# Performance work log

Hardware: AMD Instinct MI355X
Metric: run time of the kernel (lower is better)

## Reference

```python
import jax, jax.numpy as jnp
import numpy as np

IMAGE_SIZE = 224  # self.image_size; dims are all equal to this so postprocess is one bilinear resize
EPS = 1e-12      # F.normalize default eps


def setup_inputs() -> dict:
    key = jax.random.key(0)
    k1, k2 = jax.random.split(key)
    embeddings = jax.random.normal(k1, (2, 9, 256, 48, 48), dtype=jnp.float32)
    # binary class masks in {0,1}; channel 0 (background) is recomputed inside forward
    prompt_masks = jax.random.randint(k2, (2, 8, 4, 48, 48), 0, 2).astype(jnp.float32)
    dims = jnp.full((2, 1, 2), IMAGE_SIZE, dtype=jnp.int32)  # all original sizes == image_size
    return {"embeddings": embeddings, "prompt_masks": prompt_masks, "dims": dims}


def reference(embeddings, prompt_masks, dims):
    B, M, D, H, W = embeddings.shape
    HW = H * W
    q = embeddings[:, 0]            # (B, D, H, W)  query
    s = embeddings[:, 1:]           # (B, M-1, D, H, W)  supports
    # F.normalize: x / max(||x||, eps) along the feature dim
    qn = q / jnp.maximum(jnp.sqrt(jnp.sum(q * q, axis=1, keepdims=True)), EPS)
    sn = s / jnp.maximum(jnp.sqrt(jnp.sum(s * s, axis=2, keepdims=True)), EPS)

    q2 = qn.reshape(B, D, HW).transpose(0, 2, 1)              # (B, Q, D)
    s2 = sn.reshape(B, M - 1, D, HW).transpose(0, 1, 3, 2)    # (B, M1, K, D)
    sim = jnp.einsum('bqd,bmkd->bqmk', q2, s2)                # (B, Q, M1, K) cosine sims

    # nearest-resize of prompt masks to compare_size==(H,W) is identity here (same size)
    N = prompt_masks.shape[2]
    pm = prompt_masks.reshape(B, M - 1, N, HW)
    background = (pm[:, :, 1:, :].sum(axis=2) == 0).astype(sim.dtype)  # (B, M1, HW)
    pm = pm.at[:, :, 0, :].set(background)

    neg_inf = jnp.array(-jnp.inf, sim.dtype)
    logits = []
    for n in range(N):  # small fixed class count
        cm = pm[:, :, n, :][:, None]                 # (B, 1, M1, K) broadcast over Q
        masked = jnp.where(cm == 0, neg_inf, sim)    # (B, Q, M1, K)
        logits.append(masked.reshape(B, HW, -1).max(axis=-1))  # (B, Q)
    logits = jnp.stack(logits, axis=1).reshape(B, N, H, W)

    # postprocess_masks: bilinear to image_size; all original sizes == image_size so the
    # per-image second interpolate is identity and padding amounts are zero.
    out = jax.image.resize(logits, (B, N, IMAGE_SIZE, IMAGE_SIZE), method='bilinear')
    # masks[:,0][masks[:,0]==-inf] = 0  (no-op here, kept for faithfulness)
    out = out.at[:, 0].set(jnp.where(jnp.isneginf(out[:, 0]), 0.0, out[:, 0]))
    return out
```

## Files before the change

### kernel.cpp

```cpp
#include <hip/hip_runtime.h>
#include <hip/hip_bf16.h>
#include <math.h>

#define BB 2
#define MM 9
#define MS 8
#define DD 256
#define HW 2304
#define NCLS 4
#define OUTR 224

typedef float floatx4 __attribute__((ext_vector_type(4)));
typedef __bf16 bf16x8 __attribute__((ext_vector_type(8)));
typedef unsigned short ushortx8 __attribute__((ext_vector_type(8)));

__device__ __forceinline__ unsigned enc_f(float f) {
    unsigned u = __float_as_uint(f);
    return (u & 0x80000000u) ? ~u : (u | 0x80000000u);
}
__device__ __forceinline__ float dec_f(unsigned k) {
    unsigned u = (k & 0x80000000u) ? (k & 0x7FFFFFFFu) : ~k;
    return __uint_as_float(u);
}

__global__ __launch_bounds__(256) void knorm(const float* __restrict__ emb,
                                             __hip_bfloat16* __restrict__ outp,
                                             unsigned* __restrict__ enc_logits) {
    __shared__ float tile[256][33];
    __shared__ float psum[8][32];
    __shared__ float sscale[32];
    const int bm   = blockIdx.y;
    const int pix0 = blockIdx.x * 32;
    const int tid  = threadIdx.x;

    int flat = (blockIdx.y * gridDim.x + blockIdx.x) * 256 + tid;
    if (flat < BB * NCLS * HW) enc_logits[flat] = 0u;

    const float* src = emb + (size_t)bm * DD * HW + pix0;
    {
        const int dr = tid >> 3;
        const int p4 = (tid & 7) * 4;
#pragma unroll
        for (int r = 0; r < 8; ++r) {
            int d = r * 32 + dr;
            floatx4 v = *(const floatx4*)(src + (size_t)d * HW + p4);
            float* t = &tile[d][p4];
            t[0] = v[0]; t[1] = v[1]; t[2] = v[2]; t[3] = v[3];
        }
    }
    __syncthreads();
    {
        const int pc = tid & 31;
        const int dr = tid >> 5;
        float ss = 0.f;
#pragma unroll
        for (int s = 0; s < 32; ++s) {
            float v = tile[dr * 32 + s][pc];
            ss += v * v;
        }
        psum[dr][pc] = ss;
    }
    __syncthreads();
    if (tid < 32) {
        float t = 0.f;
#pragma unroll
        for (int c = 0; c < 8; ++c) t += psum[c][tid];
        sscale[tid] = 1.0f / fmaxf(sqrtf(t), 1e-12f);
    }
    __syncthreads();
    __hip_bfloat16* dst = outp + (size_t)bm * HW * DD + (size_t)pix0 * DD;
#pragma unroll
    for (int r = 0; r < 32; ++r) {
        float v = tile[tid][r] * sscale[r];
        dst[(size_t)r * DD + tid] = __float2bfloat16(v);
    }
}

__device__ __forceinline__ void gld16(const unsigned short* g, unsigned short* l) {
    __builtin_amdgcn_global_load_lds((__attribute__((address_space(1))) void*)g,
                                     (__attribute__((address_space(3))) void*)l, 16, 0, 0);
}

#define BK 64
#define REDSTRIDE 132
#define SMEM_BYTES 33792

__global__ __launch_bounds__(256, 4) void kgemm(const unsigned short* __restrict__ normed,
                                                const float* __restrict__ pm,
                                                unsigned* __restrict__ enc_logits) {
    __shared__ __attribute__((aligned(16))) unsigned char smem[SMEM_BYTES];
    unsigned short* As = (unsigned short*)smem;
    unsigned short* Bs = As + 128 * 64;
    float* red = (float*)smem;

    const int ct = blockIdx.x;
    const int rt = blockIdx.y;
    const int b  = blockIdx.z;
    const int m  = ct / 18;
    const int kt = ct % 18;

    const int tid  = threadIdx.x;
    const int lane = tid & 63;
    const int wave = tid >> 6;
    const int wr = wave >> 1, wc = wave & 1;
    const int lrow = lane & 15;
    const int quad = lane >> 4;

    const unsigned short* A  = normed + (size_t)(b * MM) * (HW * DD) + (size_t)(rt * 128) * DD;
    const unsigned short* Bp = normed + (size_t)(b * MM + 1 + m) * (HW * DD) + (size_t)(kt * 128) * DD;

    const float* pmB = pm + (size_t)(b * MS + m) * NCLS * HW;
    int mj[4];
#pragma unroll
    for (int j = 0; j < 4; ++j) {
        int kp = kt * 128 + wc * 64 + j * 16 + lrow;
        float p1 = pmB[HW + kp], p2 = pmB[2 * HW + kp], p3 = pmB[3 * HW + kp];
        mj[j] = ((p1 + p2 + p3 == 0.0f) ? 1 : 0) | (p1 != 0.0f ? 2 : 0) |
                (p2 != 0.0f ? 4 : 0) | (p3 != 0.0f ? 8 : 0);
    }

    const int srq  = lane >> 3;
    const int scol = ((lane & 7) ^ srq) * 8;

    floatx4 zero = {0.f, 0.f, 0.f, 0.f};
    floatx4 acc[4][4];
#pragma unroll
    for (int i = 0; i < 4; ++i)
#pragma unroll
        for (int j = 0; j < 4; ++j) acc[i][j] = zero;

    for (int k0 = 0; k0 < DD; k0 += BK) {
#pragma unroll
        for (int q = 0; q < 4; ++q) {
            int row = wave * 32 + q * 8 + srq;
            gld16(A  + (size_t)row * DD + k0 + scol, As + (wave * 4 + q) * 512);
            gld16(Bp + (size_t)row * DD + k0 + scol, Bs + (wave * 4 + q) * 512);
        }
        __syncthreads();
#pragma unroll
        for (int kk = 0; kk < 2; ++kk) {
            bf16x8 af[4], bfr[4];
#pragma unroll
            for (int i = 0; i < 4; ++i) {
                int ar = wr * 64 + i * 16 + lrow;
                int br = wc * 64 + i * 16 + lrow;
                int pcA = (kk * 4 + quad) ^ (ar & 7);
                int pcB = (kk * 4 + quad) ^ (br & 7);
                af[i]  = __builtin_bit_cast(bf16x8, *(const ushortx8*)(As + ar * 64 + pcA * 8));
                bfr[i] = __builtin_bit_cast(bf16x8, *(const ushortx8*)(Bs + br * 64 + pcB * 8));
            }
#pragma unroll
            for (int i = 0; i < 4; ++i)
#pragma unroll
                for (int j = 0; j < 4; ++j)
                    acc[i][j] = __builtin_amdgcn_mfma_f32_16x16x32_bf16(af[i], bfr[j], acc[i][j], 0, 0, 0);
        }
        __syncthreads();
    }

    const int col32 = wc * 16 + lrow;

#pragma unroll
    for (int p = 0; p < 2; ++p) {
        if (p) __syncthreads();
        bool bit[2][4];
#pragma unroll
        for (int nn = 0; nn < 2; ++nn) {
            int n = p * 2 + nn;
#pragma unroll
            for (int j = 0; j < 4; ++j) bit[nn][j] = (mj[j] >> n) & 1;
        }
#pragma unroll
        for (int nn = 0; nn < 2; ++nn) {
#pragma unroll
            for (int i = 0; i < 4; ++i) {
                floatx4 o;
#pragma unroll
                for (int r = 0; r < 4; ++r) {
                    float t0 = bit[nn][0] ? acc[i][0][r] : -INFINITY;
                    float t1 = bit[nn][1] ? acc[i][1][r] : -INFINITY;
                    float t2 = bit[nn][2] ? acc[i][2][r] : -INFINITY;
                    float t3 = bit[nn][3] ? acc[i][3][r] : -INFINITY;
                    o[r] = fmaxf(fmaxf(t0, t1), fmaxf(t2, t3));
                }
                int rowbase = wr * 64 + i * 16 + quad * 4;
                *(floatx4*)(red + ((size_t)(nn * 32 + col32)) * REDSTRIDE + rowbase) = o;
            }
        }
        __syncthreads();
        {
            int nn  = tid >> 7;
            int row = tid & 127;
            float v = -INFINITY;
#pragma unroll
            for (int c = 0; c < 32; ++c)
                v = fmaxf(v, red[((size_t)(nn * 32 + c)) * REDSTRIDE + row]);
            int n = p * 2 + nn;
            atomicMax(enc_logits + ((size_t)b * NCLS + n) * HW + rt * 128 + row, enc_f(v));
        }
    }
}

__global__ __launch_bounds__(256) void kresize(const unsigned* __restrict__ enc_logits,
                                               float* __restrict__ out) {
    int idx = blockIdx.x * 256 + threadIdx.x;
    if (idx >= BB * NCLS * OUTR * OUTR) return;
    int ox = idx % OUTR;
    int oy = (idx / OUTR) % OUTR;
    int bn = idx / (OUTR * OUTR);
    const unsigned* src = enc_logits + (size_t)bn * HW;
    const float inv = 48.0f / 224.0f;
    float sx = (ox + 0.5f) * inv - 0.5f;
    float sy = (oy + 0.5f) * inv - 0.5f;
    int x0 = (int)floorf(sx); float fx = sx - x0;
    int y0 = (int)floorf(sy); float fy = sy - y0;
    int x0c = min(max(x0, 0), 47), x1c = min(max(x0 + 1, 0), 47);
    int y0c = min(max(y0, 0), 47), y1c = min(max(y0 + 1, 0), 47);
    float v00 = dec_f(src[y0c * 48 + x0c]), v01 = dec_f(src[y0c * 48 + x1c]);
    float v10 = dec_f(src[y1c * 48 + x0c]), v11 = dec_f(src[y1c * 48 + x1c]);
    float v = (1.f - fy) * ((1.f - fx) * v00 + fx * v01) + fy * ((1.f - fx) * v10 + fx * v11);
    if ((bn & 3) == 0 && v == -INFINITY) v = 0.f;
    out[idx] = v;
}

extern "C" void kernel_launch(void* const* d_in, const int* in_sizes, int n_in,
                              void* d_out, int out_size, void* d_ws, size_t ws_size,
                              hipStream_t stream) {
    const float* emb = (const float*)d_in[0];
    const float* pm  = (const float*)d_in[1];
    float* out = (float*)d_out;

    char* ws = (char*)d_ws;
    const size_t normed_bytes = (size_t)BB * MM * HW * DD * 2;
    __hip_bfloat16* normed = (__hip_bfloat16*)(ws);
    unsigned*       enc    = (unsigned*)(ws + normed_bytes);

    knorm<<<dim3(HW / 32, BB * MM), 256, 0, stream>>>(emb, normed, enc);
    kgemm<<<dim3(144, 18, BB), 256, 0, stream>>>((const unsigned short*)normed, pm, enc);
    kresize<<<(BB * NCLS * OUTR * OUTR + 255) / 256, 256, 0, stream>>>(enc, out);
}
```

Measured before the change: 150.3 us.

## Double-buffer GEMM LDS tiles with BK=32 to overlap loads and MFMA

The GEMM K-loop is restructured into a two-stage software pipeline. K-tiles shrink from 64 to 32, and two LDS buffers are alternated so the asynchronous global-to-LDS load of the next tile is issued before the MFMAs on the current tile. This is meant to hide global load latency, which was previously exposed by the load-then-sync pattern. It halves the work per barrier, doubles the number of iterations, and changes the swizzle pattern to match the narrower rows.

Result: faster. 145.8 us (-3.0%).

```diff
diff --git a/kernel.cpp b/kernel.cpp
--- a/kernel.cpp
+++ b/kernel.cpp
@@ -81,7 +81,7 @@
                                      (__attribute__((address_space(3))) void*)l, 16, 0, 0);
 }
 
-#define BK 64
+#define BK 32
 #define REDSTRIDE 132
 #define SMEM_BYTES 33792
 
@@ -89,8 +89,7 @@
                                                 const float* __restrict__ pm,
                                                 unsigned* __restrict__ enc_logits) {
     __shared__ __attribute__((aligned(16))) unsigned char smem[SMEM_BYTES];
-    unsigned short* As = (unsigned short*)smem;
-    unsigned short* Bs = As + 128 * 64;
+    unsigned short* const S0 = (unsigned short*)smem;
     float* red = (float*)smem;
 
     const int ct = blockIdx.x;
@@ -119,8 +118,10 @@
                 (p2 != 0.0f ? 4 : 0) | (p3 != 0.0f ? 8 : 0);
     }
 
-    const int srq  = lane >> 3;
-    const int scol = ((lane & 7) ^ srq) * 8;
+    const int srq  = lane >> 2;
+    const int scol = ((lane & 3) ^ ((srq >> 1) & 3)) * 8;
+    const unsigned short* gA = A  + (size_t)(wave * 32 + srq) * DD + scol;
+    const unsigned short* gB = Bp + (size_t)(wave * 32 + srq) * DD + scol;
 
     floatx4 zero = {0.f, 0.f, 0.f, 0.f};
     floatx4 acc[4][4];
@@ -129,32 +130,41 @@
 #pragma unroll
         for (int j = 0; j < 4; ++j) acc[i][j] = zero;
 
-    for (int k0 = 0; k0 < DD; k0 += BK) {
-#pragma unroll
-        for (int q = 0; q < 4; ++q) {
-            int row = wave * 32 + q * 8 + srq;
-            gld16(A  + (size_t)row * DD + k0 + scol, As + (wave * 4 + q) * 512);
-            gld16(Bp + (size_t)row * DD + k0 + scol, Bs + (wave * 4 + q) * 512);
-        }
-        __syncthreads();
-#pragma unroll
-        for (int kk = 0; kk < 2; ++kk) {
-            bf16x8 af[4], bfr[4];
-#pragma unroll
-            for (int i = 0; i < 4; ++i) {
-                int ar = wr * 64 + i * 16 + lrow;
-                int br = wc * 64 + i * 16 + lrow;
-                int pcA = (kk * 4 + quad) ^ (ar & 7);
-                int pcB = (kk * 4 + quad) ^ (br & 7);
-                af[i]  = __builtin_bit_cast(bf16x8, *(const ushortx8*)(As + ar * 64 + pcA * 8));
-                bfr[i] = __builtin_bit_cast(bf16x8, *(const ushortx8*)(Bs + br * 64 + pcB * 8));
+#pragma unroll
+    for (int q = 0; q < 2; ++q) {
+        gld16(gA + (size_t)(q * 16) * DD, S0 +        (wave * 2 + q) * 512);
+        gld16(gB + (size_t)(q * 16) * DD, S0 + 4096 + (wave * 2 + q) * 512);
+    }
+    __syncthreads();
+
+    const int pc8 = (quad ^ ((lrow >> 1) & 3)) * 8;
+
+#pragma unroll
+    for (int t = 0; t < DD / BK; ++t) {
+        const int cb = t & 1;
+        unsigned short* const Ac = S0 + cb * 8192;
+        unsigned short* const Bc = Ac + 4096;
+        if (t < DD / BK - 1) {
+            unsigned short* const An = S0 + (cb ^ 1) * 8192;
+#pragma unroll
+            for (int q = 0; q < 2; ++q) {
+                gld16(gA + (size_t)(q * 16) * DD + (t + 1) * BK, An +        (wave * 2 + q) * 512);
+                gld16(gB + (size_t)(q * 16) * DD + (t + 1) * BK, An + 4096 + (wave * 2 + q) * 512);
             }
-#pragma unroll
-            for (int i = 0; i < 4; ++i)
-#pragma unroll
-                for (int j = 0; j < 4; ++j)
-                    acc[i][j] = __builtin_amdgcn_mfma_f32_16x16x32_bf16(af[i], bfr[j], acc[i][j], 0, 0, 0);
-        }
+        }
+        bf16x8 af[4], bfr[4];
+#pragma unroll
+        for (int i = 0; i < 4; ++i) {
+            int ar = wr * 64 + i * 16 + lrow;
+            int br = wc * 64 + i * 16 + lrow;
+            af[i]  = __builtin_bit_cast(bf16x8, *(const ushortx8*)(Ac + ar * 32 + pc8));
+            bfr[i] = __builtin_bit_cast(bf16x8, *(const ushortx8*)(Bc + br * 32 + pc8));
+        }
+#pragma unroll
+        for (int i = 0; i < 4; ++i)
+#pragma unroll
+            for (int j = 0; j < 4; ++j)
+                acc[i][j] = __builtin_amdgcn_mfma_f32_16x16x32_bf16(af[i], bfr[j], acc[i][j], 0, 0, 0);
         __syncthreads();
     }
 
```

## Double-buffer GEMM tiles and process three key tiles per block with register max

Applied to the files above, without the earlier changes.

Each GEMM block now handles three consecutive support-pixel tiles and keeps a running per-class max in registers. The cross-wave LDS reduction and atomicMax therefore run once per three tiles instead of once per tile. Global-to-LDS loads are double-buffered so the next K-slice is fetched while MFMAs run on the current one. In exchange the kernel uses twice the shared memory, more registers, occupancy drops to two blocks per CU, and the grid shrinks from 144 to 48 column groups.

After: 150.4 us. Within noise of the previous version (+0.1%).

```diff
diff --git a/kernel.cpp b/kernel.cpp
--- a/kernel.cpp
+++ b/kernel.cpp
@@ -81,23 +81,24 @@
                                      (__attribute__((address_space(3))) void*)l, 16, 0, 0);
 }
 
+#define NKT 3
 #define BK 64
 #define REDSTRIDE 132
-#define SMEM_BYTES 33792
-
-__global__ __launch_bounds__(256, 4) void kgemm(const unsigned short* __restrict__ normed,
+#define SMEM_BYTES 65536
+
+__global__ __launch_bounds__(256, 2) void kgemm(const unsigned short* __restrict__ normed,
                                                 const float* __restrict__ pm,
                                                 unsigned* __restrict__ enc_logits) {
     __shared__ __attribute__((aligned(16))) unsigned char smem[SMEM_BYTES];
-    unsigned short* As = (unsigned short*)smem;
-    unsigned short* Bs = As + 128 * 64;
+    unsigned short* const S = (unsigned short*)smem;
     float* red = (float*)smem;
 
-    const int ct = blockIdx.x;
+    const int gx = blockIdx.x;
     const int rt = blockIdx.y;
     const int b  = blockIdx.z;
-    const int m  = ct / 18;
-    const int kt = ct % 18;
+    const int m  = gx / 6;
+    const int cg = gx % 6;
+    const int kt0 = cg * NKT;
 
     const int tid  = threadIdx.x;
     const int lane = tid & 63;
@@ -107,20 +108,16 @@
     const int quad = lane >> 4;
 
     const unsigned short* A  = normed + (size_t)(b * MM) * (HW * DD) + (size_t)(rt * 128) * DD;
-    const unsigned short* Bp = normed + (size_t)(b * MM + 1 + m) * (HW * DD) + (size_t)(kt * 128) * DD;
-
+    const unsigned short* Bp = normed + (size_t)(b * MM + 1 + m) * (HW * DD);
     const float* pmB = pm + (size_t)(b * MS + m) * NCLS * HW;
-    int mj[4];
-#pragma unroll
-    for (int j = 0; j < 4; ++j) {
-        int kp = kt * 128 + wc * 64 + j * 16 + lrow;
-        float p1 = pmB[HW + kp], p2 = pmB[2 * HW + kp], p3 = pmB[3 * HW + kp];
-        mj[j] = ((p1 + p2 + p3 == 0.0f) ? 1 : 0) | (p1 != 0.0f ? 2 : 0) |
-                (p2 != 0.0f ? 4 : 0) | (p3 != 0.0f ? 8 : 0);
-    }
-
-    const int srq  = lane >> 3;
-    const int scol = ((lane & 7) ^ srq) * 8;
+
+    const int srow = lane >> 3;
+    const int sc   = ((lane & 7) ^ srow) * 8;
+    const unsigned short* gA = A  + (size_t)(wave * 32 + srow) * DD + sc;
+    const unsigned short* gB = Bp + (size_t)(wave * 32 + srow) * DD + sc;
+
+    const int pc0 = ((0 * 4 + quad) ^ (lrow & 7)) * 8;
+    const int pc1 = ((1 * 4 + quad) ^ (lrow & 7)) * 8;
 
     floatx4 zero = {0.f, 0.f, 0.f, 0.f};
     floatx4 acc[4][4];
@@ -129,60 +126,109 @@
 #pragma unroll
         for (int j = 0; j < 4; ++j) acc[i][j] = zero;
 
-    for (int k0 = 0; k0 < DD; k0 += BK) {
-#pragma unroll
-        for (int q = 0; q < 4; ++q) {
-            int row = wave * 32 + q * 8 + srq;
-            gld16(A  + (size_t)row * DD + k0 + scol, As + (wave * 4 + q) * 512);
-            gld16(Bp + (size_t)row * DD + k0 + scol, Bs + (wave * 4 + q) * 512);
-        }
-        __syncthreads();
-#pragma unroll
-        for (int kk = 0; kk < 2; ++kk) {
-            bf16x8 af[4], bfr[4];
-#pragma unroll
-            for (int i = 0; i < 4; ++i) {
-                int ar = wr * 64 + i * 16 + lrow;
-                int br = wc * 64 + i * 16 + lrow;
-                int pcA = (kk * 4 + quad) ^ (ar & 7);
-                int pcB = (kk * 4 + quad) ^ (br & 7);
-                af[i]  = __builtin_bit_cast(bf16x8, *(const ushortx8*)(As + ar * 64 + pcA * 8));
-                bfr[i] = __builtin_bit_cast(bf16x8, *(const ushortx8*)(Bs + br * 64 + pcB * 8));
-            }
-#pragma unroll
-            for (int i = 0; i < 4; ++i)
+    float omax[4][4][4];
+#pragma unroll
+    for (int n = 0; n < 4; ++n)
+#pragma unroll
+        for (int i = 0; i < 4; ++i)
+#pragma unroll
+            for (int r = 0; r < 4; ++r) omax[n][i][r] = -INFINITY;
+
+#define STAGE(bufN, ktS, k0S) do {                                             \
+        unsigned short* dA_ = S + (bufN) * 16384 + wave * 4 * 512;             \
+        unsigned short* dB_ = dA_ + 8192;                                      \
+        const unsigned short* sA_ = gA + (k0S);                                \
+        const unsigned short* sB_ = gB + (size_t)(ktS) * 128 * DD + (k0S);     \
+        _Pragma("unroll")                                                      \
+        for (int q_ = 0; q_ < 4; ++q_) {                                       \
+            gld16(sA_ + (size_t)(q_ * 8) * DD, dA_ + q_ * 512);                \
+            gld16(sB_ + (size_t)(q_ * 8) * DD, dB_ + q_ * 512);                \
+        }                                                                      \
+    } while (0)
+
+    STAGE(0, kt0, 0);
+    __syncthreads();
+
+    for (int ktl = 0; ktl < NKT; ++ktl) {
+        const int kt = kt0 + ktl;
+        float mp1[4], mp2[4], mp3[4];
+#pragma unroll
+        for (int j = 0; j < 4; ++j) {
+            int kp = kt * 128 + wc * 64 + j * 16 + lrow;
+            mp1[j] = pmB[HW + kp];
+            mp2[j] = pmB[2 * HW + kp];
+            mp3[j] = pmB[3 * HW + kp];
+        }
+#pragma unroll
+        for (int k0i = 0; k0i < 4; ++k0i) {
+            const int cur = k0i & 1;
+            if (!(ktl == NKT - 1 && k0i == 3)) {
+                if (k0i == 3) STAGE(cur ^ 1, kt + 1, 0);
+                else          STAGE(cur ^ 1, kt, (k0i + 1) * BK);
+            }
+            const unsigned short* Ac = S + cur * 16384;
+            const unsigned short* Bc = Ac + 8192;
+#pragma unroll
+            for (int kk = 0; kk < 2; ++kk) {
+                const int pc = kk ? pc1 : pc0;
+                bf16x8 af[4], bfr[4];
+#pragma unroll
+                for (int i = 0; i < 4; ++i) {
+                    int ar = wr * 64 + i * 16 + lrow;
+                    int br = wc * 64 + i * 16 + lrow;
+                    af[i]  = __builtin_bit_cast(bf16x8, *(const ushortx8*)(Ac + ar * 64 + pc));
+                    bfr[i] = __builtin_bit_cast(bf16x8, *(const ushortx8*)(Bc + br * 64 + pc));
+                }
+#pragma unroll
+                for (int i = 0; i < 4; ++i)
+#pragma unroll
+                    for (int j = 0; j < 4; ++j)
+                        acc[i][j] = __builtin_amdgcn_mfma_f32_16x16x32_bf16(af[i], bfr[j], acc[i][j], 0, 0, 0);
+            }
+            if (k0i == 3) {
+                int mj[4];
 #pragma unroll
                 for (int j = 0; j < 4; ++j)
-                    acc[i][j] = __builtin_amdgcn_mfma_f32_16x16x32_bf16(af[i], bfr[j], acc[i][j], 0, 0, 0);
-        }
-        __syncthreads();
-    }
+                    mj[j] = ((mp1[j] + mp2[j] + mp3[j] == 0.0f) ? 1 : 0) | (mp1[j] != 0.0f ? 2 : 0) |
+                            (mp2[j] != 0.0f ? 4 : 0) | (mp3[j] != 0.0f ? 8 : 0);
+#pragma unroll
+                for (int n = 0; n < 4; ++n) {
+                    bool b0 = (mj[0] >> n) & 1, b1 = (mj[1] >> n) & 1;
+                    bool b2 = (mj[2] >> n) & 1, b3 = (mj[3] >> n) & 1;
+#pragma unroll
+                    for (int i = 0; i < 4; ++i)
+#pragma unroll
+                        for (int r = 0; r < 4; ++r) {
+                            float t0 = b0 ? acc[i][0][r] : -INFINITY;
+                            float t1 = b1 ? acc[i][1][r] : -INFINITY;
+                            float t2 = b2 ? acc[i][2][r] : -INFINITY;
+                            float t3 = b3 ? acc[i][3][r] : -INFINITY;
+                            omax[n][i][r] = fmaxf(omax[n][i][r],
+                                                  fmaxf(fmaxf(t0, t1), fmaxf(t2, t3)));
+                        }
+                }
+#pragma unroll
+                for (int i = 0; i < 4; ++i)
+#pragma unroll
+                    for (int j = 0; j < 4; ++j) acc[i][j] = zero;
+            }
+            __syncthreads();
+        }
+    }
+#undef STAGE
 
     const int col32 = wc * 16 + lrow;
-
 #pragma unroll
     for (int p = 0; p < 2; ++p) {
         if (p) __syncthreads();
-        bool bit[2][4];
 #pragma unroll
         for (int nn = 0; nn < 2; ++nn) {
             int n = p * 2 + nn;
 #pragma unroll
-            for (int j = 0; j < 4; ++j) bit[nn][j] = (mj[j] >> n) & 1;
-        }
-#pragma unroll
-        for (int nn = 0; nn < 2; ++nn) {
-#pragma unroll
             for (int i = 0; i < 4; ++i) {
                 floatx4 o;
 #pragma unroll
-                for (int r = 0; r < 4; ++r) {
-                    float t0 = bit[nn][0] ? acc[i][0][r] : -INFINITY;
-                    float t1 = bit[nn][1] ? acc[i][1][r] : -INFINITY;
-                    float t2 = bit[nn][2] ? acc[i][2][r] : -INFINITY;
-                    float t3 = bit[nn][3] ? acc[i][3][r] : -INFINITY;
-                    o[r] = fmaxf(fmaxf(t0, t1), fmaxf(t2, t3));
-                }
+                for (int r = 0; r < 4; ++r) o[r] = omax[n][i][r];
                 int rowbase = wr * 64 + i * 16 + quad * 4;
                 *(floatx4*)(red + ((size_t)(nn * 32 + col32)) * REDSTRIDE + rowbase) = o;
             }
@@ -236,6 +282,6 @@
     unsigned*       enc    = (unsigned*)(ws + normed_bytes);
 
     knorm<<<dim3(HW / 32, BB * MM), 256, 0, stream>>>(emb, normed, enc);
-    kgemm<<<dim3(144, 18, BB), 256, 0, stream>>>((const unsigned short*)normed, pm, enc);
+    kgemm<<<dim3(48, 18, BB), 256, 0, stream>>>((const unsigned short*)normed, pm, enc);
     kresize<<<(BB * NCLS * OUTR * OUTR + 255) / 256, 256, 0, stream>>>(enc, out);
 }
```
